# Performance work log

Measured on AMD Instinct MI355X. Metric: run time of the kernel, lower is better.

The kernel has to match this reference:

```python
import jax, jax.numpy as jnp
import numpy as np

B, N, C = 8, 1025, 768  # batch, tokens (1 CLS + 32*32 patches), channels
H = 12                  # heads
D = C // H              # head dim = 64
EPS = 1e-6

def _rot(x):
    # stack([-x[..., 1::2], x[..., ::2]], -1).reshape(x.shape)
    return jnp.stack([-x[..., 1::2], x[..., ::2]], axis=-1).reshape(x.shape)

def apply_rot_embed_cat(x, emb):
    # emb: [N-1, 2*D] = concat(sin, cos); x: [B, H, N-1, D]
    sin, cos = jnp.split(emb, 2, axis=-1)
    return x * cos + _rot(x) * sin

def setup_inputs() -> dict:
    key = jax.random.key(0)
    ks = jax.random.split(key, 8)
    s = 0.02
    return {
        "x": jax.random.normal(ks[0], (B, N, C), jnp.float32),
        "rope": jax.random.normal(ks[1], (N - 1, 2 * D), jnp.float32),
        "w_qkv": jax.random.normal(ks[2], (C, 3 * C), jnp.float32) * s,
        "q_bias": jax.random.normal(ks[3], (C,), jnp.float32) * s,
        "v_bias": jax.random.normal(ks[4], (C,), jnp.float32) * s,
        "gamma": jnp.ones((C,), jnp.float32),
        "beta": jnp.zeros((C,), jnp.float32),
        "w_proj": jax.random.normal(ks[5], (C, C), jnp.float32) * s,
        "b_proj": jnp.zeros((C,), jnp.float32),
    }

def reference(x, rope, w_qkv, q_bias, v_bias, gamma, beta, w_proj, b_proj):
    scale = D ** (-0.5)
    qkv_bias = jnp.concatenate([q_bias, jnp.zeros_like(q_bias), v_bias], axis=0)
    qkv = x @ w_qkv + qkv_bias  # [B, N, 3C]
    qkv = qkv.reshape(B, N, 3, H, D).transpose(2, 0, 3, 1, 4)  # [3, B, H, N, D]
    q, k, v = qkv[0], qkv[1], qkv[2]
    # RoPE on non-CLS tokens only
    q = jnp.concatenate([q[:, :, :1], apply_rot_embed_cat(q[:, :, 1:], rope)], axis=2)
    k = jnp.concatenate([k[:, :, :1], apply_rot_embed_cat(k[:, :, 1:], rope)], axis=2)
    attn = jnp.einsum('bhqd,bhkd->bhqk', q * scale, k)
    attn = jax.nn.softmax(attn, axis=-1)
    y = jnp.einsum('bhqk,bhkd->bhqd', attn, v)
    y = y.transpose(0, 2, 1, 3).reshape(B, N, C)
    # LayerNorm
    mu = jnp.mean(y, axis=-1, keepdims=True)
    var = jnp.mean(jnp.square(y - mu), axis=-1, keepdims=True)
    y = (y - mu) * jax.lax.rsqrt(var + EPS) * gamma + beta
    return y @ w_proj + b_proj
```

## Files before the change

kernel.cpp:

```cpp
#include <hip/hip_runtime.h>

typedef __bf16 bf16_t;
typedef __bf16 bf16x8 __attribute__((ext_vector_type(8)));
typedef float f32x4 __attribute__((ext_vector_type(4)));
typedef float f32x16 __attribute__((ext_vector_type(16)));
typedef unsigned short u16;
typedef unsigned int u32;

#define NTOK 1025
#define NPAD 1056
#define NPADV 1088
#define BH   96
#define CDIM 768

__device__ __forceinline__ u16 f2bf(float f) {
  union { float f; unsigned u; } v; v.f = f;
  unsigned r = v.u + 0x7fffu + ((v.u >> 16) & 1u);
  return (u16)(r >> 16);
}
__device__ __forceinline__ float bf2f(u16 h) {
  union { unsigned u; float f; } v; v.u = ((unsigned)h) << 16; return v.f;
}
__device__ __forceinline__ u32 cvtpk(float lo, float hi) {
  u32 r; asm("v_cvt_pk_bf16_f32 %0, %1, %2" : "=v"(r) : "v"(lo), "v"(hi)); return r;
}
__device__ __forceinline__ void gld16(const void* g, void* l) {
  __builtin_amdgcn_global_load_lds(
      (const __attribute__((address_space(1))) unsigned*)g,
      (__attribute__((address_space(3))) unsigned*)l, 16, 0, 0);
}

__global__ void conv_x(const float4* __restrict__ in, u16* __restrict__ out, int n4) {
  int i = blockIdx.x * blockDim.x + threadIdx.x;
  if (i < n4) {
    float4 f = in[i];
    ushort4 o; o.x = f2bf(f.x); o.y = f2bf(f.y); o.z = f2bf(f.z); o.w = f2bf(f.w);
    *(ushort4*)&out[i * 4] = o;
  }
}

__global__ __launch_bounds__(256) void transp(const float* __restrict__ in,
                                              u16* __restrict__ out, int K, int N) {
  __shared__ float tile[32][33];
  int n0 = blockIdx.x * 32, k0 = blockIdx.y * 32;
  int tx = threadIdx.x & 31, ty = threadIdx.x >> 5;
#pragma unroll
  for (int i = 0; i < 4; ++i)
    tile[ty + i * 8][tx] = in[(k0 + ty + i * 8) * N + n0 + tx];
  __syncthreads();
#pragma unroll
  for (int i = 0; i < 4; ++i)
    out[(n0 + ty + i * 8) * K + k0 + tx] = f2bf(tile[tx][ty + i * 8]);
}

__global__ __launch_bounds__(256) void qkv_gemm(
    const u16* __restrict__ A, const u16* __restrict__ Bt,
    const float* __restrict__ qbias, const float* __restrict__ vbias,
    u16* __restrict__ qkp, u16* __restrict__ vt) {
  const int M = 8200, K = 768, NB = 18;
  __shared__ u16 As[2][8192], Bs[2][8192];
  int tau0 = blockIdx.x;
  int xcd = tau0 & 7, pos = tau0 >> 3;
  int tau = (xcd < 2) ? xcd * 147 + pos : 294 + (xcd - 2) * 146 + pos;
  int bx = tau % NB, by = tau / NB;
  int m0 = by * 128, n0 = bx * 128;
  int t = threadIdx.x;
  int lane = t & 63, wave = t >> 6;
  int ln = lane & 15, hi = lane >> 4;
  int wr = wave >> 1, wc = wave & 1;
  int swz = (ln & 7) << 4;
  f32x4 acc[4][4] = {};
  int trow = t >> 3;
  int tcolb = (t & 7) * 16;
  int scol = ((tcolb ^ ((trow & 7) << 4)) >> 1);

  auto stage = [&](int buf, int k0) {
#pragma unroll
    for (int c = 0; c < 4; ++c) {
      int arow = m0 + c * 32 + trow;
      gld16(&A[(size_t)arow * K + k0 + scol], &As[buf][c * 2048 + t * 8]);
      int brow = n0 + c * 32 + trow;
      gld16(&Bt[(size_t)brow * K + k0 + scol], &Bs[buf][c * 2048 + t * 8]);
    }
  };

  stage(0, 0);
  for (int it = 0; it < 12; ++it) {
    int cur = it & 1;
    if (it < 11) {
      stage(cur ^ 1, (it + 1) * 64);
      asm volatile("s_waitcnt vmcnt(8)" ::: "memory");
    } else {
      asm volatile("s_waitcnt vmcnt(0)" ::: "memory");
    }
    __builtin_amdgcn_s_barrier();
    asm volatile("" ::: "memory");
#pragma unroll
    for (int kk = 0; kk < 2; ++kk) {
      bf16x8 af[4], bfr[4];
#pragma unroll
      for (int i = 0; i < 4; ++i)
        af[i] = *(const bf16x8*)((const char*)&As[cur][(wr * 64 + i * 16 + ln) * 64]
                                 + ((kk * 64 + hi * 16) ^ swz));
#pragma unroll
      for (int j = 0; j < 4; ++j)
        bfr[j] = *(const bf16x8*)((const char*)&Bs[cur][(wc * 64 + j * 16 + ln) * 64]
                                  + ((kk * 64 + hi * 16) ^ swz));
#pragma unroll
      for (int i = 0; i < 4; ++i)
#pragma unroll
        for (int j = 0; j < 4; ++j)
          acc[i][j] = __builtin_amdgcn_mfma_f32_16x16x32_bf16(af[i], bfr[j], acc[i][j], 0, 0, 0);
    }
    asm volatile("" ::: "memory");
    __builtin_amdgcn_s_barrier();
  }

  if (n0 < 1536) {
#pragma unroll
    for (int i = 0; i < 4; ++i) {
      int mrow = m0 + wr * 64 + i * 16 + hi * 4;
#pragma unroll
      for (int j = 0; j < 4; ++j) {
        int col = n0 + wc * 64 + j * 16 + ln;
        float bv = (col < CDIM) ? qbias[col] : 0.f;
#pragma unroll
        for (int r = 0; r < 4; ++r) {
          int m = mrow + r;
          if (m < M) qkp[(size_t)m * 1536 + col] = f2bf(acc[i][j][r] + bv);
        }
      }
    }
  } else {
#pragma unroll
    for (int i = 0; i < 4; ++i) {
      int mrow = m0 + wr * 64 + i * 16 + hi * 4;
#pragma unroll
      for (int j = 0; j < 4; ++j) {
        int col = n0 + wc * 64 + j * 16 + ln;
        int c = col - 1536;
        int h = c >> 6, d = c & 63;
        float bv = vbias[c];
#pragma unroll
        for (int r = 0; r < 4; ++r) {
          int m = mrow + r;
          if (m < M) {
            int b = m / NTOK;
            int n = m - b * NTOK;
            vt[((size_t)((b * 12 + h) * 64 + d)) * NPADV + n] = f2bf(acc[i][j][r] + bv);
          }
        }
      }
    }
  }
}

__global__ __launch_bounds__(256) void rope_scatter(
    const u16* __restrict__ qkp, const float* __restrict__ rope,
    u16* __restrict__ q, u16* __restrict__ k) {
  int m = blockIdx.x;
  int b = m / NTOK, n = m - b * NTOK;
  const u16* row = qkp + (size_t)m * 1536;
  const float scale = 0.125f * 1.4426950408889634f;
  int t = threadIdx.x;
#pragma unroll
  for (int it = 0; it < 3; ++it) {
    int e = t + it * 256;
    int part = (e >= 384);
    int pp = e - part * 384;
    int h = pp >> 5, d = (pp & 31) * 2;
    u32 pr = *(const u32*)&row[e * 2];
    float v0 = bf2f((u16)(pr & 0xffff)), v1 = bf2f((u16)(pr >> 16));
    float o0 = v0, o1 = v1;
    if (n > 0) {
      const float* rp = rope + (size_t)(n - 1) * 128 + d;
      float s0 = rp[0], s1 = rp[1], c0 = rp[64], c1 = rp[65];
      o0 = v0 * c0 - v1 * s0;
      o1 = v1 * c1 + v0 * s1;
    }
    if (part == 0) { o0 *= scale; o1 *= scale; }
    u32 ov = (u32)f2bf(o0) | ((u32)f2bf(o1) << 16);
    u16* dst = (part == 0 ? q : k) + ((size_t)((b * 12 + h) * NPAD + n)) * 64 + d;
    *(u32*)dst = ov;
  }
}

__global__ __launch_bounds__(256) void flash_attn(
    const u16* __restrict__ q, const u16* __restrict__ k,
    const u16* __restrict__ vt, u16* __restrict__ y) {
  __shared__ u16 smem[2][8192];
  int f = blockIdx.x;
  int xcd = f & 7, idx = f >> 3;
  int bh = xcd * 12 + idx / 9;
  int qt = idx - (idx / 9) * 9;
  int t = threadIdx.x, lane = t & 63, w = t >> 6;
  int lq = lane & 31, h2 = lane >> 5;
  int q0 = qt * 128 + w * 32;
  bool active = (q0 < NTOK);
  int qrow = q0 + lq; if (qrow > NTOK - 1) qrow = NTOK - 1;

  const u16* qp = q + ((size_t)(bh * NPAD + qrow)) * 64;
  bf16x8 qf[4];
#pragma unroll
  for (int s = 0; s < 4; ++s)
    qf[s] = *(const bf16x8*)&qp[s * 16 + h2 * 8];

  f32x16 acc[2] = {};
  float l = 0.f;

  const size_t kbase = (size_t)bh * NPAD * 64;
  const size_t vbase = (size_t)bh * 64 * NPADV;

  auto stage = [&](int buf, int kt) {
    int t16 = t * 16;
#pragma unroll
    for (int j = 0; j < 4; ++j) {
      int off = j * 4096 + t16;
      int off2 = off & 8191;
      int row = off2 >> 7;
      int col = off2 & 127;
      int scol = col ^ ((row & 7) << 4);
      const u16* src = (j < 2)
          ? &k[kbase + (size_t)(kt + row) * 64 + (scol >> 1)]
          : &vt[vbase + (size_t)row * NPADV + kt + (scol >> 1)];
      gld16(src, (char*)&smem[buf][0] + off);
    }
  };

  stage(0, 0);
  asm volatile("s_waitcnt vmcnt(0)" ::: "memory");
  __syncthreads();

  for (int it = 0; it < 17; ++it) {
    int kt = it * 64;
    int cur = it & 1;
    if (it < 16) stage(cur ^ 1, kt + 64);

    if (active) {
      const char* kb = (const char*)&smem[cur][0];
      f32x16 sc[2] = {};
      __builtin_amdgcn_s_setprio(1);
#pragma unroll
      for (int c = 0; c < 2; ++c) {
        int krow = c * 32 + lq;
#pragma unroll
        for (int s = 0; s < 4; ++s) {
          int kcol = (s * 32 + h2 * 16) ^ ((lane & 7) << 4);
          bf16x8 kf = *(const bf16x8*)(kb + krow * 128 + kcol);
          sc[c] = __builtin_amdgcn_mfma_f32_32x32x16_bf16(kf, qf[s], sc[c], 0, 0, 0);
        }
      }
      __builtin_amdgcn_s_setprio(0);
      float p[2][16];
#pragma unroll
      for (int c = 0; c < 2; ++c)
#pragma unroll
        for (int r = 0; r < 16; ++r)
          p[c][r] = __builtin_amdgcn_exp2f(sc[c][r]);
      if (it == 16) {
#pragma unroll
        for (int c = 0; c < 2; ++c)
#pragma unroll
          for (int r = 0; r < 16; ++r) {
            int kk = kt + c * 32 + (r & 3) + 8 * (r >> 2) + 4 * h2;
            if (kk >= NTOK) p[c][r] = 0.f;
          }
      }
      float rs = 0.f;
#pragma unroll
      for (int c = 0; c < 2; ++c)
#pragma unroll
        for (int r = 0; r < 16; ++r) rs += p[c][r];
      l += rs;
      bf16x8 frag[4];
#pragma unroll
      for (int c = 0; c < 2; ++c) {
        u32 pk[8];
#pragma unroll
        for (int i = 0; i < 8; ++i) pk[i] = cvtpk(p[c][2 * i], p[c][2 * i + 1]);
        u32 x0 = __shfl_xor(pk[0], 32, 64), x1 = __shfl_xor(pk[1], 32, 64);
        u32 x2 = __shfl_xor(pk[2], 32, 64), x3 = __shfl_xor(pk[3], 32, 64);
        u32 x4 = __shfl_xor(pk[4], 32, 64), x5 = __shfl_xor(pk[5], 32, 64);
        u32 x6 = __shfl_xor(pk[6], 32, 64), x7 = __shfl_xor(pk[7], 32, 64);
        union { u32 u[4]; bf16x8 v; } u0, u1;
        u0.u[0] = h2 ? x2 : pk[0];  u0.u[1] = h2 ? x3 : pk[1];
        u0.u[2] = h2 ? pk[2] : x0;  u0.u[3] = h2 ? pk[3] : x1;
        u1.u[0] = h2 ? x6 : pk[4];  u1.u[1] = h2 ? x7 : pk[5];
        u1.u[2] = h2 ? pk[6] : x4;  u1.u[3] = h2 ? pk[7] : x5;
        frag[c * 2] = u0.v; frag[c * 2 + 1] = u1.v;
      }
      __builtin_amdgcn_s_setprio(1);
#pragma unroll
      for (int hf = 0; hf < 2; ++hf) {
        int vrow = hf * 32 + lq;
#pragma unroll
        for (int s = 0; s < 4; ++s) {
          int vcol = (s * 32 + h2 * 16) ^ ((lane & 7) << 4);
          bf16x8 vf = *(const bf16x8*)(kb + 8192 + vrow * 128 + vcol);
          acc[hf] = __builtin_amdgcn_mfma_f32_32x32x16_bf16(vf, frag[s], acc[hf], 0, 0, 0);
        }
      }
      __builtin_amdgcn_s_setprio(0);
    }
    asm volatile("s_waitcnt vmcnt(0)" ::: "memory");
    __syncthreads();
  }

  int row = q0 + lq;
  if (active && row < NTOK) {
    float lt = l + __shfl_xor(l, 32, 64);
    float inv = 1.f / lt;
    int b = bh / 12, h = bh - b * 12;
    u16* yr = y + ((size_t)(b * NTOK + row)) * CDIM + h * 64;
#pragma unroll
    for (int hf = 0; hf < 2; ++hf)
#pragma unroll
      for (int g = 0; g < 4; ++g) {
        int d0 = hf * 32 + 8 * g + 4 * h2;
        ushort4 o;
        o.x = f2bf(acc[hf][g * 4 + 0] * inv);
        o.y = f2bf(acc[hf][g * 4 + 1] * inv);
        o.z = f2bf(acc[hf][g * 4 + 2] * inv);
        o.w = f2bf(acc[hf][g * 4 + 3] * inv);
        *(ushort4*)&yr[d0] = o;
      }
  }
}

__global__ __launch_bounds__(256) void lnorm(const u16* __restrict__ y,
                                             const float* __restrict__ gamma,
                                             const float* __restrict__ beta,
                                             u16* __restrict__ out) {
  int row = blockIdx.x;
  const u16* yr = y + (size_t)row * CDIM;
  int t = threadIdx.x;
  float v[3];
  float s = 0.f, s2 = 0.f;
#pragma unroll
  for (int i = 0; i < 3; ++i) {
    v[i] = bf2f(yr[t + 256 * i]);
    s += v[i]; s2 += v[i] * v[i];
  }
#pragma unroll
  for (int msk = 1; msk < 64; msk <<= 1) {
    s  += __shfl_xor(s, msk, 64);
    s2 += __shfl_xor(s2, msk, 64);
  }
  __shared__ float ws[8];
  int w = t >> 6, lane = t & 63;
  if (lane == 0) { ws[w] = s; ws[4 + w] = s2; }
  __syncthreads();
  s = ws[0] + ws[1] + ws[2] + ws[3];
  s2 = ws[4] + ws[5] + ws[6] + ws[7];
  float mu = s * (1.f / 768.f);
  float var = s2 * (1.f / 768.f) - mu * mu;
  float rstd = rsqrtf(var + 1e-6f);
#pragma unroll
  for (int i = 0; i < 3; ++i) {
    int c = t + 256 * i;
    out[(size_t)row * CDIM + c] = f2bf((v[i] - mu) * rstd * gamma[c] + beta[c]);
  }
}

__global__ __launch_bounds__(256) void proj_gemm(
    const u16* __restrict__ A, const u16* __restrict__ Bt,
    const float* __restrict__ bias, float* __restrict__ out) {
  const int M = 8200, K = 768, NB = 6;
  __shared__ u16 As[2][8192], Bs[2][8192];
  int tau0 = blockIdx.x;
  int xcd = tau0 & 7, pos = tau0 >> 3;
  int tau = (xcd < 6) ? xcd * 49 + pos : 294 + (xcd - 6) * 48 + pos;
  int bx = tau % NB, by = tau / NB;
  int m0 = by * 128, n0 = bx * 128;
  int t = threadIdx.x;
  int lane = t & 63, wave = t >> 6;
  int ln = lane & 15, hi = lane >> 4;
  int wr = wave >> 1, wc = wave & 1;
  int swz = (ln & 7) << 4;
  f32x4 acc[4][4] = {};
  int trow = t >> 3;
  int tcolb = (t & 7) * 16;
  int scol = ((tcolb ^ ((trow & 7) << 4)) >> 1);

  auto stage = [&](int buf, int k0) {
#pragma unroll
    for (int c = 0; c < 4; ++c) {
      int arow = m0 + c * 32 + trow;
      gld16(&A[(size_t)arow * K + k0 + scol], &As[buf][c * 2048 + t * 8]);
      int brow = n0 + c * 32 + trow;
      gld16(&Bt[(size_t)brow * K + k0 + scol], &Bs[buf][c * 2048 + t * 8]);
    }
  };

  stage(0, 0);
  for (int it = 0; it < 12; ++it) {
    int cur = it & 1;
    if (it < 11) {
      stage(cur ^ 1, (it + 1) * 64);
      asm volatile("s_waitcnt vmcnt(8)" ::: "memory");
    } else {
      asm volatile("s_waitcnt vmcnt(0)" ::: "memory");
    }
    __builtin_amdgcn_s_barrier();
    asm volatile("" ::: "memory");
#pragma unroll
    for (int kk = 0; kk < 2; ++kk) {
      bf16x8 af[4], bfr[4];
#pragma unroll
      for (int i = 0; i < 4; ++i)
        af[i] = *(const bf16x8*)((const char*)&As[cur][(wr * 64 + i * 16 + ln) * 64]
                                 + ((kk * 64 + hi * 16) ^ swz));
#pragma unroll
      for (int j = 0; j < 4; ++j)
        bfr[j] = *(const bf16x8*)((const char*)&Bs[cur][(wc * 64 + j * 16 + ln) * 64]
                                  + ((kk * 64 + hi * 16) ^ swz));
#pragma unroll
      for (int i = 0; i < 4; ++i)
#pragma unroll
        for (int j = 0; j < 4; ++j)
          acc[i][j] = __builtin_amdgcn_mfma_f32_16x16x32_bf16(af[i], bfr[j], acc[i][j], 0, 0, 0);
    }
    asm volatile("" ::: "memory");
    __builtin_amdgcn_s_barrier();
  }
#pragma unroll
  for (int i = 0; i < 4; ++i) {
    int mrow = m0 + wr * 64 + i * 16 + hi * 4;
#pragma unroll
    for (int j = 0; j < 4; ++j) {
      int col = n0 + wc * 64 + j * 16 + ln;
      float bv = bias[col];
#pragma unroll
      for (int r = 0; r < 4; ++r) {
        int m = mrow + r;
        if (m < M) out[(size_t)m * CDIM + col] = acc[i][j][r] + bv;
      }
    }
  }
}

extern "C" void kernel_launch(void* const* d_in, const int* in_sizes, int n_in,
                              void* d_out, int out_size, void* d_ws, size_t ws_size,
                              hipStream_t stream) {
  const float* x      = (const float*)d_in[0];
  const float* rope   = (const float*)d_in[1];
  const float* w_qkv  = (const float*)d_in[2];
  const float* q_bias = (const float*)d_in[3];
  const float* v_bias = (const float*)d_in[4];
  const float* gamma  = (const float*)d_in[5];
  const float* beta   = (const float*)d_in[6];
  const float* w_proj = (const float*)d_in[7];
  const float* b_proj = (const float*)d_in[8];
  float* out = (float*)d_out;

  char* ws = (char*)d_ws;
  u16* xb    = (u16*)(ws);
  u16* qbuf  = (u16*)(ws);
  u16* ylb   = (u16*)(ws);
  u16* wqkvt = (u16*)(ws + 12976128);
  u16* kbuf  = (u16*)(ws + 12976128);
  u16* qkp   = (u16*)(ws + 25952256);
  u16* ybf   = (u16*)(ws + 25952256);
  u16* vtbuf = (u16*)(ws + 51142656);
  u16* wprjt = (u16*)(ws + 64512000);

  hipMemsetAsync(vtbuf, 0, 13369344, stream);

  conv_x<<<(1574400 + 255) / 256, 256, 0, stream>>>((const float4*)x, xb, 1574400);
  transp<<<dim3(2304 / 32, 768 / 32), 256, 0, stream>>>(w_qkv, wqkvt, 768, 2304);
  transp<<<dim3(768 / 32, 768 / 32), 256, 0, stream>>>(w_proj, wprjt, 768, 768);

  qkv_gemm<<<dim3(1170), 256, 0, stream>>>(xb, wqkvt, q_bias, v_bias, qkp, vtbuf);
  rope_scatter<<<dim3(8200), 256, 0, stream>>>(qkp, rope, qbuf, kbuf);
  flash_attn<<<dim3(864), 256, 0, stream>>>(qbuf, kbuf, vtbuf, ybf);
  lnorm<<<8200, 256, 0, stream>>>(ybf, gamma, beta, ylb);
  proj_gemm<<<dim3(390), 256, 0, stream>>>(ylb, wprjt, b_proj, out);
}
```

Baseline: 188.5 us.

## Triple-buffer QKV and projection GEMMs with smaller K tiles and MFMA priority

Both GEMM kernels move from double-buffered 64-wide K tiles to triple-buffered 32-wide K tiles, which cuts LDS per block from 64KB to 48KB and raises the occupancy hint to 3 blocks per CU. Loads are issued two stages ahead, the LDS swizzle is reworked for the narrower tiles, and s_setprio is raised around the MFMA block. The goal is to hide global-load latency and fit more resident blocks. The cost is twice as many barriers per K pass and a tighter register budget.

```diff
diff --git a/kernel.cpp b/kernel.cpp
--- a/kernel.cpp
+++ b/kernel.cpp
@@ -53,12 +53,12 @@
     out[(n0 + ty + i * 8) * K + k0 + tx] = f2bf(tile[tx][ty + i * 8]);
 }
 
-__global__ __launch_bounds__(256) void qkv_gemm(
+__global__ __launch_bounds__(256, 3) void qkv_gemm(
     const u16* __restrict__ A, const u16* __restrict__ Bt,
     const float* __restrict__ qbias, const float* __restrict__ vbias,
     u16* __restrict__ qkp, u16* __restrict__ vt) {
   const int M = 8200, K = 768, NB = 18;
-  __shared__ u16 As[2][8192], Bs[2][8192];
+  __shared__ u16 As[3][4096], Bs[3][4096];
   int tau0 = blockIdx.x;
   int xcd = tau0 & 7, pos = tau0 >> 3;
   int tau = (xcd < 2) ? xcd * 147 + pos : 294 + (xcd - 2) * 146 + pos;
@@ -68,50 +68,49 @@
   int lane = t & 63, wave = t >> 6;
   int ln = lane & 15, hi = lane >> 4;
   int wr = wave >> 1, wc = wave & 1;
-  int swz = (ln & 7) << 4;
   f32x4 acc[4][4] = {};
-  int trow = t >> 3;
-  int tcolb = (t & 7) * 16;
-  int scol = ((tcolb ^ ((trow & 7) << 4)) >> 1);
-
-  auto stage = [&](int buf, int k0) {
-#pragma unroll
-    for (int c = 0; c < 4; ++c) {
-      int arow = m0 + c * 32 + trow;
-      gld16(&A[(size_t)arow * K + k0 + scol], &As[buf][c * 2048 + t * 8]);
-      int brow = n0 + c * 32 + trow;
-      gld16(&Bt[(size_t)brow * K + k0 + scol], &Bs[buf][c * 2048 + t * 8]);
+  int srow = t >> 2;
+  int off0 = t * 16;
+  int ssrc = ((t & 3) * 16) ^ ((srow & 3) << 4);
+  int rswz = (hi * 16) ^ ((ln & 3) << 4);
+
+  auto stage = [&](int buf, int kt) {
+    int k0 = kt * 32 + (ssrc >> 1);
+#pragma unroll
+    for (int q2 = 0; q2 < 2; ++q2) {
+      int row = q2 * 64 + srow;
+      gld16(&A[(size_t)(m0 + row) * K + k0], (char*)&As[buf][0] + q2 * 4096 + off0);
+      gld16(&Bt[(size_t)(n0 + row) * K + k0], (char*)&Bs[buf][0] + q2 * 4096 + off0);
     }
   };
 
   stage(0, 0);
-  for (int it = 0; it < 12; ++it) {
-    int cur = it & 1;
-    if (it < 11) {
-      stage(cur ^ 1, (it + 1) * 64);
+  stage(1, 1);
+  for (int ph = 0; ph < 24; ++ph) {
+    int buf = ph % 3;
+    if (ph < 22) {
+      stage((ph + 2) % 3, ph + 2);
       asm volatile("s_waitcnt vmcnt(8)" ::: "memory");
+    } else if (ph == 22) {
+      asm volatile("s_waitcnt vmcnt(4)" ::: "memory");
     } else {
       asm volatile("s_waitcnt vmcnt(0)" ::: "memory");
     }
     __builtin_amdgcn_s_barrier();
     asm volatile("" ::: "memory");
-#pragma unroll
-    for (int kk = 0; kk < 2; ++kk) {
-      bf16x8 af[4], bfr[4];
-#pragma unroll
-      for (int i = 0; i < 4; ++i)
-        af[i] = *(const bf16x8*)((const char*)&As[cur][(wr * 64 + i * 16 + ln) * 64]
-                                 + ((kk * 64 + hi * 16) ^ swz));
+    bf16x8 af[4], bfr[4];
+#pragma unroll
+    for (int i = 0; i < 4; ++i) {
+      af[i]  = *(const bf16x8*)((const char*)&As[buf][0] + (wr * 64 + i * 16 + ln) * 64 + rswz);
+      bfr[i] = *(const bf16x8*)((const char*)&Bs[buf][0] + (wc * 64 + i * 16 + ln) * 64 + rswz);
+    }
+    __builtin_amdgcn_s_setprio(1);
+#pragma unroll
+    for (int i = 0; i < 4; ++i)
 #pragma unroll
       for (int j = 0; j < 4; ++j)
-        bfr[j] = *(const bf16x8*)((const char*)&Bs[cur][(wc * 64 + j * 16 + ln) * 64]
-                                  + ((kk * 64 + hi * 16) ^ swz));
-#pragma unroll
-      for (int i = 0; i < 4; ++i)
-#pragma unroll
-        for (int j = 0; j < 4; ++j)
-          acc[i][j] = __builtin_amdgcn_mfma_f32_16x16x32_bf16(af[i], bfr[j], acc[i][j], 0, 0, 0);
-    }
+        acc[i][j] = __builtin_amdgcn_mfma_f32_16x16x32_bf16(af[i], bfr[j], acc[i][j], 0, 0, 0);
+    __builtin_amdgcn_s_setprio(0);
     asm volatile("" ::: "memory");
     __builtin_amdgcn_s_barrier();
   }
@@ -362,11 +361,11 @@
   }
 }
 
-__global__ __launch_bounds__(256) void proj_gemm(
+__global__ __launch_bounds__(256, 3) void proj_gemm(
     const u16* __restrict__ A, const u16* __restrict__ Bt,
     const float* __restrict__ bias, float* __restrict__ out) {
   const int M = 8200, K = 768, NB = 6;
-  __shared__ u16 As[2][8192], Bs[2][8192];
+  __shared__ u16 As[3][4096], Bs[3][4096];
   int tau0 = blockIdx.x;
   int xcd = tau0 & 7, pos = tau0 >> 3;
   int tau = (xcd < 6) ? xcd * 49 + pos : 294 + (xcd - 6) * 48 + pos;
@@ -376,50 +375,49 @@
   int lane = t & 63, wave = t >> 6;
   int ln = lane & 15, hi = lane >> 4;
   int wr = wave >> 1, wc = wave & 1;
-  int swz = (ln & 7) << 4;
   f32x4 acc[4][4] = {};
-  int trow = t >> 3;
-  int tcolb = (t & 7) * 16;
-  int scol = ((tcolb ^ ((trow & 7) << 4)) >> 1);
-
-  auto stage = [&](int buf, int k0) {
-#pragma unroll
-    for (int c = 0; c < 4; ++c) {
-      int arow = m0 + c * 32 + trow;
-      gld16(&A[(size_t)arow * K + k0 + scol], &As[buf][c * 2048 + t * 8]);
-      int brow = n0 + c * 32 + trow;
-      gld16(&Bt[(size_t)brow * K + k0 + scol], &Bs[buf][c * 2048 + t * 8]);
+  int srow = t >> 2;
+  int off0 = t * 16;
+  int ssrc = ((t & 3) * 16) ^ ((srow & 3) << 4);
+  int rswz = (hi * 16) ^ ((ln & 3) << 4);
+
+  auto stage = [&](int buf, int kt) {
+    int k0 = kt * 32 + (ssrc >> 1);
+#pragma unroll
+    for (int q2 = 0; q2 < 2; ++q2) {
+      int row = q2 * 64 + srow;
+      gld16(&A[(size_t)(m0 + row) * K + k0], (char*)&As[buf][0] + q2 * 4096 + off0);
+      gld16(&Bt[(size_t)(n0 + row) * K + k0], (char*)&Bs[buf][0] + q2 * 4096 + off0);
     }
   };
 
   stage(0, 0);
-  for (int it = 0; it < 12; ++it) {
-    int cur = it & 1;
-    if (it < 11) {
-      stage(cur ^ 1, (it + 1) * 64);
+  stage(1, 1);
+  for (int ph = 0; ph < 24; ++ph) {
+    int buf = ph % 3;
+    if (ph < 22) {
+      stage((ph + 2) % 3, ph + 2);
       asm volatile("s_waitcnt vmcnt(8)" ::: "memory");
+    } else if (ph == 22) {
+      asm volatile("s_waitcnt vmcnt(4)" ::: "memory");
     } else {
       asm volatile("s_waitcnt vmcnt(0)" ::: "memory");
     }
     __builtin_amdgcn_s_barrier();
     asm volatile("" ::: "memory");
-#pragma unroll
-    for (int kk = 0; kk < 2; ++kk) {
-      bf16x8 af[4], bfr[4];
-#pragma unroll
-      for (int i = 0; i < 4; ++i)
-        af[i] = *(const bf16x8*)((const char*)&As[cur][(wr * 64 + i * 16 + ln) * 64]
-                                 + ((kk * 64 + hi * 16) ^ swz));
+    bf16x8 af[4], bfr[4];
+#pragma unroll
+    for (int i = 0; i < 4; ++i) {
+      af[i]  = *(const bf16x8*)((const char*)&As[buf][0] + (wr * 64 + i * 16 + ln) * 64 + rswz);
+      bfr[i] = *(const bf16x8*)((const char*)&Bs[buf][0] + (wc * 64 + i * 16 + ln) * 64 + rswz);
+    }
+    __builtin_amdgcn_s_setprio(1);
+#pragma unroll
+    for (int i = 0; i < 4; ++i)
 #pragma unroll
       for (int j = 0; j < 4; ++j)
-        bfr[j] = *(const bf16x8*)((const char*)&Bs[cur][(wc * 64 + j * 16 + ln) * 64]
-                                  + ((kk * 64 + hi * 16) ^ swz));
-#pragma unroll
-      for (int i = 0; i < 4; ++i)
-#pragma unroll
-        for (int j = 0; j < 4; ++j)
-          acc[i][j] = __builtin_amdgcn_mfma_f32_16x16x32_bf16(af[i], bfr[j], acc[i][j], 0, 0, 0);
-    }
+        acc[i][j] = __builtin_amdgcn_mfma_f32_16x16x32_bf16(af[i], bfr[j], acc[i][j], 0, 0, 0);
+    __builtin_amdgcn_s_setprio(0);
     asm volatile("" ::: "memory");
     __builtin_amdgcn_s_barrier();
   }
```

Measured after the change: 198.3 us. +5.2%, slower.

## Fuse RoPE into QKV GEMM epilogue, split V GEMM, single-buffer GEMM loop

Applied to the files above, without the earlier changes.

Splits the QKV GEMM into a Q/K kernel that computes transposed tiles and applies bias, RoPE and scale in its epilogue, writing q/k directly, plus a separate V kernel writing transposed V. This removes the rope_scatter kernel, the intermediate qkp round trip and the vt memset, by switching to an [h][b*N] layout padded to MPAD. The shared K-loop drops double buffering for a single buffer with a full wait, and adds setprio around the MFMAs. proj_gemm uses the transposed MFMA form for vectorized float4 stores. The loss of load/compute overlap in the GEMMs may cost some time, and the flash kernel now reads keys across batch boundaries within the padded layout.

```diff
diff --git a/kernel.cpp b/kernel.cpp
--- a/kernel.cpp
+++ b/kernel.cpp
@@ -8,9 +8,8 @@
 typedef unsigned int u32;
 
 #define NTOK 1025
-#define NPAD 1056
-#define NPADV 1088
-#define BH   96
+#define MTOT 8200
+#define MPAD 8448
 #define CDIM 768
 
 __device__ __forceinline__ u16 f2bf(float f) {
@@ -53,135 +52,153 @@
     out[(n0 + ty + i * 8) * K + k0 + tx] = f2bf(tile[tx][ty + i * 8]);
 }
 
-__global__ __launch_bounds__(256) void qkv_gemm(
+template <bool TRANS>
+__device__ __forceinline__ void kloop128(const u16* __restrict__ A, const u16* __restrict__ Bt,
+                                         int m0, int n0, u16* As, u16* Bs, int t,
+                                         f32x4 (*acc)[4]) {
+  const int K = 768;
+  int lane = t & 63, wave = t >> 6;
+  int ln = lane & 15, hi = lane >> 4;
+  int wr = wave >> 1, wc = wave & 1;
+  int swz = (ln & 7) << 4;
+  int trow = t >> 3;
+  int tcolb = (t & 7) * 16;
+  int scol = ((tcolb ^ ((trow & 7) << 4)) >> 1);
+
+  for (int k0 = 0; k0 < K; k0 += 64) {
+#pragma unroll
+    for (int c = 0; c < 4; ++c) {
+      gld16(&A[(size_t)(m0 + c * 32 + trow) * K + k0 + scol], &As[c * 2048 + t * 8]);
+      gld16(&Bt[(size_t)(n0 + c * 32 + trow) * K + k0 + scol], &Bs[c * 2048 + t * 8]);
+    }
+    asm volatile("s_waitcnt vmcnt(0)" ::: "memory");
+    __builtin_amdgcn_s_barrier();
+    asm volatile("" ::: "memory");
+#pragma unroll
+    for (int kk = 0; kk < 2; ++kk) {
+      bf16x8 af[4], bfr[4];
+#pragma unroll
+      for (int i = 0; i < 4; ++i)
+        af[i] = *(const bf16x8*)((const char*)&As[(wr * 64 + i * 16 + ln) * 64]
+                                 + ((kk * 64 + hi * 16) ^ swz));
+#pragma unroll
+      for (int j = 0; j < 4; ++j)
+        bfr[j] = *(const bf16x8*)((const char*)&Bs[(wc * 64 + j * 16 + ln) * 64]
+                                  + ((kk * 64 + hi * 16) ^ swz));
+      __builtin_amdgcn_s_setprio(1);
+#pragma unroll
+      for (int x = 0; x < 4; ++x)
+#pragma unroll
+        for (int y = 0; y < 4; ++y)
+          acc[x][y] = TRANS
+              ? __builtin_amdgcn_mfma_f32_16x16x32_bf16(bfr[x], af[y], acc[x][y], 0, 0, 0)
+              : __builtin_amdgcn_mfma_f32_16x16x32_bf16(af[x], bfr[y], acc[x][y], 0, 0, 0);
+      __builtin_amdgcn_s_setprio(0);
+    }
+    asm volatile("" ::: "memory");
+    __builtin_amdgcn_s_barrier();
+  }
+}
+
+__global__ __launch_bounds__(256) void qkv_gemm_t(
     const u16* __restrict__ A, const u16* __restrict__ Bt,
-    const float* __restrict__ qbias, const float* __restrict__ vbias,
-    u16* __restrict__ qkp, u16* __restrict__ vt) {
-  const int M = 8200, K = 768, NB = 18;
-  __shared__ u16 As[2][8192], Bs[2][8192];
+    const float* __restrict__ qbias, const float* __restrict__ rope,
+    u16* __restrict__ q, u16* __restrict__ k) {
+  const int NB = 12;
+  __shared__ u16 As[8192], Bs[8192];
   int tau0 = blockIdx.x;
   int xcd = tau0 & 7, pos = tau0 >> 3;
-  int tau = (xcd < 2) ? xcd * 147 + pos : 294 + (xcd - 2) * 146 + pos;
+  int tau = (xcd < 4) ? xcd * 98 + pos : 392 + (xcd - 4) * 97 + pos;
   int bx = tau % NB, by = tau / NB;
   int m0 = by * 128, n0 = bx * 128;
   int t = threadIdx.x;
   int lane = t & 63, wave = t >> 6;
   int ln = lane & 15, hi = lane >> 4;
   int wr = wave >> 1, wc = wave & 1;
-  int swz = (ln & 7) << 4;
+
   f32x4 acc[4][4] = {};
-  int trow = t >> 3;
-  int tcolb = (t & 7) * 16;
-  int scol = ((tcolb ^ ((trow & 7) << 4)) >> 1);
-
-  auto stage = [&](int buf, int k0) {
-#pragma unroll
-    for (int c = 0; c < 4; ++c) {
-      int arow = m0 + c * 32 + trow;
-      gld16(&A[(size_t)arow * K + k0 + scol], &As[buf][c * 2048 + t * 8]);
-      int brow = n0 + c * 32 + trow;
-      gld16(&Bt[(size_t)brow * K + k0 + scol], &Bs[buf][c * 2048 + t * 8]);
-    }
-  };
-
-  stage(0, 0);
-  for (int it = 0; it < 12; ++it) {
-    int cur = it & 1;
-    if (it < 11) {
-      stage(cur ^ 1, (it + 1) * 64);
-      asm volatile("s_waitcnt vmcnt(8)" ::: "memory");
-    } else {
-      asm volatile("s_waitcnt vmcnt(0)" ::: "memory");
-    }
-    __builtin_amdgcn_s_barrier();
-    asm volatile("" ::: "memory");
-#pragma unroll
-    for (int kk = 0; kk < 2; ++kk) {
-      bf16x8 af[4], bfr[4];
-#pragma unroll
-      for (int i = 0; i < 4; ++i)
-        af[i] = *(const bf16x8*)((const char*)&As[cur][(wr * 64 + i * 16 + ln) * 64]
-                                 + ((kk * 64 + hi * 16) ^ swz));
-#pragma unroll
-      for (int j = 0; j < 4; ++j)
-        bfr[j] = *(const bf16x8*)((const char*)&Bs[cur][(wc * 64 + j * 16 + ln) * 64]
-                                  + ((kk * 64 + hi * 16) ^ swz));
-#pragma unroll
-      for (int i = 0; i < 4; ++i)
-#pragma unroll
-        for (int j = 0; j < 4; ++j)
-          acc[i][j] = __builtin_amdgcn_mfma_f32_16x16x32_bf16(af[i], bfr[j], acc[i][j], 0, 0, 0);
-    }
-    asm volatile("" ::: "memory");
-    __builtin_amdgcn_s_barrier();
-  }
-
-  if (n0 < 1536) {
-#pragma unroll
-    for (int i = 0; i < 4; ++i) {
-      int mrow = m0 + wr * 64 + i * 16 + hi * 4;
+  kloop128<true>(A, Bt, m0, n0, As, Bs, t, acc);
+
+  const float scale = 0.125f * 1.4426950408889634f;
+#pragma unroll
+  for (int ii = 0; ii < 4; ++ii) {
+    int m = m0 + wr * 64 + ii * 16 + ln;
+    if (m < MTOT) {
+      int b = m / NTOK;
+      int n = m - b * NTOK;
+      const float* rp = rope + (size_t)(n - 1) * 128;
+#pragma unroll
+      for (int jj = 0; jj < 4; ++jj) {
+        int c4 = n0 + wc * 64 + jj * 16 + hi * 4;
+        int part = (c4 >= CDIM) ? 1 : 0;
+        int cc = c4 - part * CDIM;
+        int h = cc >> 6, d4 = cc & 63;
+        float v0 = acc[jj][ii][0], v1 = acc[jj][ii][1];
+        float v2 = acc[jj][ii][2], v3 = acc[jj][ii][3];
+        if (part == 0) {
+          float4 qb = *(const float4*)(qbias + cc);
+          v0 += qb.x; v1 += qb.y; v2 += qb.z; v3 += qb.w;
+        }
+        float o0, o1, o2, o3;
+        if (n > 0) {
+          float4 sn = *(const float4*)(rp + d4);
+          float4 cs = *(const float4*)(rp + 64 + d4);
+          o0 = v0 * cs.x - v1 * sn.x;
+          o1 = v1 * cs.y + v0 * sn.y;
+          o2 = v2 * cs.z - v3 * sn.z;
+          o3 = v3 * cs.w + v2 * sn.w;
+        } else { o0 = v0; o1 = v1; o2 = v2; o3 = v3; }
+        if (part == 0) { o0 *= scale; o1 *= scale; o2 *= scale; o3 *= scale; }
+        uint2 w; w.x = cvtpk(o0, o1); w.y = cvtpk(o2, o3);
+        u16* dst = (part ? k : q) + ((size_t)(h * MPAD + m)) * 64 + d4;
+        *(uint2*)dst = w;
+      }
+    }
+  }
+}
+
+__global__ __launch_bounds__(256) void qkv_gemm_v(
+    const u16* __restrict__ A, const u16* __restrict__ Bt,
+    const float* __restrict__ vbias, u16* __restrict__ vt) {
+  const int NB = 6;
+  __shared__ u16 As[8192], Bs[8192];
+  int tau0 = blockIdx.x;
+  int xcd = tau0 & 7, pos = tau0 >> 3;
+  int tau = (xcd < 6) ? xcd * 49 + pos : 294 + (xcd - 6) * 48 + pos;
+  int bx = tau % NB, by = tau / NB;
+  int m0 = by * 128, n0 = 1536 + bx * 128;
+  int t = threadIdx.x;
+  int lane = t & 63, wave = t >> 6;
+  int ln = lane & 15, hi = lane >> 4;
+  int wr = wave >> 1, wc = wave & 1;
+
+  f32x4 acc[4][4] = {};
+  kloop128<false>(A, Bt, m0, n0, As, Bs, t, acc);
+
+#pragma unroll
+  for (int i = 0; i < 4; ++i) {
+    int mrow = m0 + wr * 64 + i * 16 + hi * 4;
+    if (mrow < MTOT) {
+      bool full = (mrow + 3 < MTOT);
 #pragma unroll
       for (int j = 0; j < 4; ++j) {
-        int col = n0 + wc * 64 + j * 16 + ln;
-        float bv = (col < CDIM) ? qbias[col] : 0.f;
-#pragma unroll
-        for (int r = 0; r < 4; ++r) {
-          int m = mrow + r;
-          if (m < M) qkp[(size_t)m * 1536 + col] = f2bf(acc[i][j][r] + bv);
+        int cv = n0 - 1536 + wc * 64 + j * 16 + ln;
+        int h = cv >> 6, d = cv & 63;
+        float vb = vbias[cv];
+        float v0 = acc[i][j][0] + vb, v1 = acc[i][j][1] + vb;
+        float v2 = acc[i][j][2] + vb, v3 = acc[i][j][3] + vb;
+        u16* dst = vt + ((size_t)(h * 64 + d)) * MPAD + mrow;
+        if (full) {
+          uint2 w; w.x = cvtpk(v0, v1); w.y = cvtpk(v2, v3);
+          *(uint2*)dst = w;
+        } else {
+          float vv[4] = {v0, v1, v2, v3};
+#pragma unroll
+          for (int r = 0; r < 4; ++r)
+            if (mrow + r < MTOT) dst[r] = f2bf(vv[r]);
         }
       }
     }
-  } else {
-#pragma unroll
-    for (int i = 0; i < 4; ++i) {
-      int mrow = m0 + wr * 64 + i * 16 + hi * 4;
-#pragma unroll
-      for (int j = 0; j < 4; ++j) {
-        int col = n0 + wc * 64 + j * 16 + ln;
-        int c = col - 1536;
-        int h = c >> 6, d = c & 63;
-        float bv = vbias[c];
-#pragma unroll
-        for (int r = 0; r < 4; ++r) {
-          int m = mrow + r;
-          if (m < M) {
-            int b = m / NTOK;
-            int n = m - b * NTOK;
-            vt[((size_t)((b * 12 + h) * 64 + d)) * NPADV + n] = f2bf(acc[i][j][r] + bv);
-          }
-        }
-      }
-    }
-  }
-}
-
-__global__ __launch_bounds__(256) void rope_scatter(
-    const u16* __restrict__ qkp, const float* __restrict__ rope,
-    u16* __restrict__ q, u16* __restrict__ k) {
-  int m = blockIdx.x;
-  int b = m / NTOK, n = m - b * NTOK;
-  const u16* row = qkp + (size_t)m * 1536;
-  const float scale = 0.125f * 1.4426950408889634f;
-  int t = threadIdx.x;
-#pragma unroll
-  for (int it = 0; it < 3; ++it) {
-    int e = t + it * 256;
-    int part = (e >= 384);
-    int pp = e - part * 384;
-    int h = pp >> 5, d = (pp & 31) * 2;
-    u32 pr = *(const u32*)&row[e * 2];
-    float v0 = bf2f((u16)(pr & 0xffff)), v1 = bf2f((u16)(pr >> 16));
-    float o0 = v0, o1 = v1;
-    if (n > 0) {
-      const float* rp = rope + (size_t)(n - 1) * 128 + d;
-      float s0 = rp[0], s1 = rp[1], c0 = rp[64], c1 = rp[65];
-      o0 = v0 * c0 - v1 * s0;
-      o1 = v1 * c1 + v0 * s1;
-    }
-    if (part == 0) { o0 *= scale; o1 *= scale; }
-    u32 ov = (u32)f2bf(o0) | ((u32)f2bf(o1) << 16);
-    u16* dst = (part == 0 ? q : k) + ((size_t)((b * 12 + h) * NPAD + n)) * 64 + d;
-    *(u32*)dst = ov;
   }
 }
 
@@ -193,13 +210,17 @@
   int xcd = f & 7, idx = f >> 3;
   int bh = xcd * 12 + idx / 9;
   int qt = idx - (idx / 9) * 9;
+  int b = bh / 12, h = bh - b * 12;
   int t = threadIdx.x, lane = t & 63, w = t >> 6;
   int lq = lane & 31, h2 = lane >> 5;
   int q0 = qt * 128 + w * 32;
   bool active = (q0 < NTOK);
   int qrow = q0 + lq; if (qrow > NTOK - 1) qrow = NTOK - 1;
 
-  const u16* qp = q + ((size_t)(bh * NPAD + qrow)) * 64;
+  const size_t kbase = ((size_t)h * MPAD + (size_t)b * NTOK) * 64;
+  const size_t vbase = (size_t)h * 64 * MPAD + (size_t)b * NTOK;
+
+  const u16* qp = q + kbase + (size_t)qrow * 64;
   bf16x8 qf[4];
 #pragma unroll
   for (int s = 0; s < 4; ++s)
@@ -207,9 +228,6 @@
 
   f32x16 acc[2] = {};
   float l = 0.f;
-
-  const size_t kbase = (size_t)bh * NPAD * 64;
-  const size_t vbase = (size_t)bh * 64 * NPADV;
 
   auto stage = [&](int buf, int kt) {
     int t16 = t * 16;
@@ -222,7 +240,7 @@
       int scol = col ^ ((row & 7) << 4);
       const u16* src = (j < 2)
           ? &k[kbase + (size_t)(kt + row) * 64 + (scol >> 1)]
-          : &vt[vbase + (size_t)row * NPADV + kt + (scol >> 1)];
+          : &vt[vbase + (size_t)row * MPAD + kt + (scol >> 1)];
       gld16(src, (char*)&smem[buf][0] + off);
     }
   };
@@ -310,7 +328,6 @@
   if (active && row < NTOK) {
     float lt = l + __shfl_xor(l, 32, 64);
     float inv = 1.f / lt;
-    int b = bh / 12, h = bh - b * 12;
     u16* yr = y + ((size_t)(b * NTOK + row)) * CDIM + h * 64;
 #pragma unroll
     for (int hf = 0; hf < 2; ++hf)
@@ -365,8 +382,8 @@
 __global__ __launch_bounds__(256) void proj_gemm(
     const u16* __restrict__ A, const u16* __restrict__ Bt,
     const float* __restrict__ bias, float* __restrict__ out) {
-  const int M = 8200, K = 768, NB = 6;
-  __shared__ u16 As[2][8192], Bs[2][8192];
+  const int NB = 6;
+  __shared__ u16 As[8192], Bs[8192];
   int tau0 = blockIdx.x;
   int xcd = tau0 & 7, pos = tau0 >> 3;
   int tau = (xcd < 6) ? xcd * 49 + pos : 294 + (xcd - 6) * 48 + pos;
@@ -376,64 +393,25 @@
   int lane = t & 63, wave = t >> 6;
   int ln = lane & 15, hi = lane >> 4;
   int wr = wave >> 1, wc = wave & 1;
-  int swz = (ln & 7) << 4;
+
   f32x4 acc[4][4] = {};
-  int trow = t >> 3;
-  int tcolb = (t & 7) * 16;
-  int scol = ((tcolb ^ ((trow & 7) << 4)) >> 1);
-
-  auto stage = [&](int buf, int k0) {
-#pragma unroll
-    for (int c = 0; c < 4; ++c) {
-      int arow = m0 + c * 32 + trow;
-      gld16(&A[(size_t)arow * K + k0 + scol], &As[buf][c * 2048 + t * 8]);
-      int brow = n0 + c * 32 + trow;
-      gld16(&Bt[(size_t)brow * K + k0 + scol], &Bs[buf][c * 2048 + t * 8]);
-    }
-  };
-
-  stage(0, 0);
-  for (int it = 0; it < 12; ++it) {
-    int cur = it & 1;
-    if (it < 11) {
-      stage(cur ^ 1, (it + 1) * 64);
-      asm volatile("s_waitcnt vmcnt(8)" ::: "memory");
-    } else {
-      asm volatile("s_waitcnt vmcnt(0)" ::: "memory");
-    }
-    __builtin_amdgcn_s_barrier();
-    asm volatile("" ::: "memory");
-#pragma unroll
-    for (int kk = 0; kk < 2; ++kk) {
-      bf16x8 af[4], bfr[4];
-#pragma unroll
-      for (int i = 0; i < 4; ++i)
-        af[i] = *(const bf16x8*)((const char*)&As[cur][(wr * 64 + i * 16 + ln) * 64]
-                                 + ((kk * 64 + hi * 16) ^ swz));
-#pragma unroll
-      for (int j = 0; j < 4; ++j)
-        bfr[j] = *(const bf16x8*)((const char*)&Bs[cur][(wc * 64 + j * 16 + ln) * 64]
-                                  + ((kk * 64 + hi * 16) ^ swz));
-#pragma unroll
-      for (int i = 0; i < 4; ++i)
-#pragma unroll
-        for (int j = 0; j < 4; ++j)
-          acc[i][j] = __builtin_amdgcn_mfma_f32_16x16x32_bf16(af[i], bfr[j], acc[i][j], 0, 0, 0);
-    }
-    asm volatile("" ::: "memory");
-    __builtin_amdgcn_s_barrier();
-  }
-#pragma unroll
-  for (int i = 0; i < 4; ++i) {
-    int mrow = m0 + wr * 64 + i * 16 + hi * 4;
-#pragma unroll
-    for (int j = 0; j < 4; ++j) {
-      int col = n0 + wc * 64 + j * 16 + ln;
-      float bv = bias[col];
-#pragma unroll
-      for (int r = 0; r < 4; ++r) {
-        int m = mrow + r;
-        if (m < M) out[(size_t)m * CDIM + col] = acc[i][j][r] + bv;
+  kloop128<true>(A, Bt, m0, n0, As, Bs, t, acc);
+
+#pragma unroll
+  for (int ii = 0; ii < 4; ++ii) {
+    int m = m0 + wr * 64 + ii * 16 + ln;
+    if (m < MTOT) {
+      float* dr = out + (size_t)m * CDIM;
+#pragma unroll
+      for (int jj = 0; jj < 4; ++jj) {
+        int c4 = n0 + wc * 64 + jj * 16 + hi * 4;
+        float4 bv = *(const float4*)(bias + c4);
+        float4 o;
+        o.x = acc[jj][ii][0] + bv.x;
+        o.y = acc[jj][ii][1] + bv.y;
+        o.z = acc[jj][ii][2] + bv.z;
+        o.w = acc[jj][ii][3] + bv.w;
+        *(float4*)(dr + c4) = o;
       }
     }
   }
@@ -455,24 +433,21 @@
 
   char* ws = (char*)d_ws;
   u16* xb    = (u16*)(ws);
-  u16* qbuf  = (u16*)(ws);
-  u16* ylb   = (u16*)(ws);
+  u16* ybf   = (u16*)(ws);
   u16* wqkvt = (u16*)(ws + 12976128);
-  u16* kbuf  = (u16*)(ws + 12976128);
-  u16* qkp   = (u16*)(ws + 25952256);
-  u16* ybf   = (u16*)(ws + 25952256);
-  u16* vtbuf = (u16*)(ws + 51142656);
-  u16* wprjt = (u16*)(ws + 64512000);
-
-  hipMemsetAsync(vtbuf, 0, 13369344, stream);
+  u16* wprjt = (u16*)(ws + 16515072);
+  u16* qbuf  = (u16*)(ws + 17694720);
+  u16* ylb   = (u16*)(ws + 17694720);
+  u16* kbuf  = (u16*)(ws + 30670848);
+  u16* vtg   = (u16*)(ws + 43646976);
 
   conv_x<<<(1574400 + 255) / 256, 256, 0, stream>>>((const float4*)x, xb, 1574400);
   transp<<<dim3(2304 / 32, 768 / 32), 256, 0, stream>>>(w_qkv, wqkvt, 768, 2304);
   transp<<<dim3(768 / 32, 768 / 32), 256, 0, stream>>>(w_proj, wprjt, 768, 768);
 
-  qkv_gemm<<<dim3(1170), 256, 0, stream>>>(xb, wqkvt, q_bias, v_bias, qkp, vtbuf);
-  rope_scatter<<<dim3(8200), 256, 0, stream>>>(qkp, rope, qbuf, kbuf);
-  flash_attn<<<dim3(864), 256, 0, stream>>>(qbuf, kbuf, vtbuf, ybf);
+  qkv_gemm_t<<<dim3(780), 256, 0, stream>>>(xb, wqkvt, q_bias, rope, qbuf, kbuf);
+  qkv_gemm_v<<<dim3(390), 256, 0, stream>>>(xb, wqkvt, v_bias, vtg);
+  flash_attn<<<dim3(864), 256, 0, stream>>>(qbuf, kbuf, vtg, ybf);
   lnorm<<<8200, 256, 0, stream>>>(ybf, gamma, beta, ylb);
   proj_gemm<<<dim3(390), 256, 0, stream>>>(ylb, wprjt, b_proj, out);
 }
```

After: 169.5 us. 1.11x faster.
